# Kernel optimization log

Measured on AMD Instinct MI355X. Metric: run time of the kernel, lower is better.

Reference implementation:

```python
import jax, jax.numpy as jnp
import numpy as np

R = 1          # radius
EPS = 0.01
K = 2 * R + 1  # box kernel size


def boxfilter(x):
    """Replication-pad by R, then depthwise KxK mean filter (groups=C)."""
    xp = jnp.pad(x, ((0, 0), (0, 0), (R, R), (R, R)), mode='edge')
    c = x.shape[1]
    k = jnp.full((c, 1, K, K), 1.0 / (K * K), dtype=x.dtype)
    return jax.lax.conv_general_dilated(
        xp, k, window_strides=(1, 1), padding='VALID',
        feature_group_count=c,
        dimension_numbers=('NCHW', 'OIHW', 'NCHW'))


def _interp_axis(arr, n_in, n_out, axis):
    # bilinear with align_corners=True along one axis
    pos = jnp.linspace(0.0, n_in - 1.0, n_out)
    i0 = jnp.floor(pos).astype(jnp.int32)
    i1 = jnp.minimum(i0 + 1, n_in - 1)
    t = (pos - i0).astype(arr.dtype)
    a0 = jnp.take(arr, i0, axis=axis)
    a1 = jnp.take(arr, i1, axis=axis)
    shp = [1] * arr.ndim
    shp[axis] = n_out
    t = t.reshape(shp)
    return a0 * (1 - t) + a1 * t


def upsample_bilinear(x, H, W):
    _, _, h, w = x.shape
    x = _interp_axis(x, h, H, 2)
    x = _interp_axis(x, w, W, 3)
    return x


def setup_inputs() -> dict:
    key = jax.random.key(0)
    k1, k2, k3 = jax.random.split(key, 3)
    x_lr = jax.random.uniform(k1, (4, 3, 512, 512), dtype=jnp.float32)
    y_lr = jax.random.uniform(k2, (4, 3, 512, 512), dtype=jnp.float32)
    x_hr = jax.random.uniform(k3, (4, 3, 2048, 2048), dtype=jnp.float32)
    return {'x_lr': x_lr, 'y_lr': y_lr, 'x_hr': x_hr}


def reference(x_lr, y_lr, x_hr):
    H, W = x_hr.shape[2], x_hr.shape[3]
    mean_x = boxfilter(x_lr)
    mean_y = boxfilter(y_lr)
    cov_xy = boxfilter(x_lr * y_lr) - mean_x * mean_y
    var_x = boxfilter(x_lr * x_lr) - mean_x * mean_x
    A = cov_xy / (var_x + EPS)
    b = mean_y - A * mean_x
    mean_A = upsample_bilinear(boxfilter(A), H, W)
    mean_b = upsample_bilinear(boxfilter(b), H, W)
    res = jnp.clip(mean_A * x_hr + mean_b, 0.0, 255.0)
    return res.astype(jnp.float32)
```

## Files before the change

kernel.cpp:

```cpp
#include <hip/hip_runtime.h>

#define RAD   1
#define EPS_F 0.01f
#define LR_H  512
#define LR_W  512
#define HR_H  2048
#define HR_W  2048
#define NC    12

#define LR_PLANE (LR_H * LR_W)
#define HR_PLANE (HR_H * HR_W)
#define LR_TOTAL (NC * LR_PLANE)
#define HR_TOTAL (NC * HR_PLANE)

__global__ void __launch_bounds__(256) k_compute_Ab(
    const float* __restrict__ x, const float* __restrict__ y,
    float* __restrict__ A, float* __restrict__ b) {
    int idx = blockIdx.x * blockDim.x + threadIdx.x;
    if (idx >= LR_TOTAL) return;
    int w = idx & (LR_W - 1);
    int h = (idx >> 9) & (LR_H - 1);
    int plane = idx >> 18;
    const float* xp = x + (size_t)plane * LR_PLANE;
    const float* yp = y + (size_t)plane * LR_PLANE;

    float sx = 0.f, sy = 0.f, sxy = 0.f, sxx = 0.f;
#pragma unroll
    for (int di = -1; di <= 1; ++di) {
        int hh = min(max(h + di, 0), LR_H - 1);
        int rowoff = hh * LR_W;
#pragma unroll
        for (int dj = -1; dj <= 1; ++dj) {
            int ww = min(max(w + dj, 0), LR_W - 1);
            float xv = xp[rowoff + ww];
            float yv = yp[rowoff + ww];
            sx  += xv;
            sy  += yv;
            sxy += xv * yv;
            sxx += xv * xv;
        }
    }
    const float inv9 = 1.0f / 9.0f;
    float mx  = sx  * inv9;
    float my  = sy  * inv9;
    float cov = sxy * inv9 - mx * my;
    float var = sxx * inv9 - mx * mx;
    float Av  = cov / (var + EPS_F);
    float bv  = my - Av * mx;
    A[idx] = Av;
    b[idx] = bv;
}

__global__ void __launch_bounds__(256) k_box_Ab(
    const float* __restrict__ A, const float* __restrict__ b,
    float* __restrict__ mA, float* __restrict__ mb) {
    int idx = blockIdx.x * blockDim.x + threadIdx.x;
    if (idx >= LR_TOTAL) return;
    int w = idx & (LR_W - 1);
    int h = (idx >> 9) & (LR_H - 1);
    int plane = idx >> 18;
    const float* Ap = A + (size_t)plane * LR_PLANE;
    const float* bp = b + (size_t)plane * LR_PLANE;

    float sA = 0.f, sB = 0.f;
#pragma unroll
    for (int di = -1; di <= 1; ++di) {
        int hh = min(max(h + di, 0), LR_H - 1);
        int rowoff = hh * LR_W;
#pragma unroll
        for (int dj = -1; dj <= 1; ++dj) {
            int ww = min(max(w + dj, 0), LR_W - 1);
            sA += Ap[rowoff + ww];
            sB += bp[rowoff + ww];
        }
    }
    const float inv9 = 1.0f / 9.0f;
    mA[idx] = sA * inv9;
    mb[idx] = sB * inv9;
}

__global__ void __launch_bounds__(256) k_upsample_fuse(
    const float* __restrict__ mA, const float* __restrict__ mb,
    const float* __restrict__ xhr, float* __restrict__ out) {
    __shared__ float hA[513];
    __shared__ float hb[513];

    int bid = blockIdx.x;
    int i     = bid & (HR_H - 1);
    int plane = bid >> 11;

    const float scale = (float)(LR_H - 1) / (float)(HR_H - 1);

    float ph = i * scale;
    int   i0 = (int)ph;
    int   i1 = min(i0 + 1, LR_H - 1);
    float th = ph - (float)i0;
    float omh = 1.0f - th;

    const float* Ap = mA + (size_t)plane * LR_PLANE;
    const float* bp = mb + (size_t)plane * LR_PLANE;
    int tid = threadIdx.x;

    for (int c = tid; c < 513; c += 256) {
        int col = min(c, LR_W - 1);
        float a0 = Ap[i0 * LR_W + col];
        float a1 = Ap[i1 * LR_W + col];
        float b0 = bp[i0 * LR_W + col];
        float b1 = bp[i1 * LR_W + col];
        hA[c] = a0 * omh + a1 * th;
        hb[c] = b0 * omh + b1 * th;
    }
    __syncthreads();

    const float* xrow = xhr + (size_t)plane * HR_PLANE + (size_t)i * HR_W;
    float*       orow = out + (size_t)plane * HR_PLANE + (size_t)i * HR_W;

#pragma unroll
    for (int g = 0; g < 2; ++g) {
        int j = (tid + g * 256) * 4;
        const float4 xv = *(const float4*)(xrow + j);
        float xin[4] = {xv.x, xv.y, xv.z, xv.w};
        float r[4];
#pragma unroll
        for (int k = 0; k < 4; ++k) {
            float pw = (float)(j + k) * scale;
            int   j0 = (int)pw;
            float tw = pw - (float)j0;
            float omw = 1.0f - tw;
            float a  = hA[j0] * omw + hA[j0 + 1] * tw;
            float bb = hb[j0] * omw + hb[j0 + 1] * tw;
            float v  = a * xin[k] + bb;
            r[k] = fminf(fmaxf(v, 0.0f), 255.0f);
        }
        float4 o;
        o.x = r[0]; o.y = r[1]; o.z = r[2]; o.w = r[3];
        *(float4*)(orow + j) = o;
    }
}

extern "C" void kernel_launch(void* const* d_in, const int* in_sizes, int n_in,
                              void* d_out, int out_size, void* d_ws, size_t ws_size,
                              hipStream_t stream) {
    const float* x_lr = (const float*)d_in[0];
    const float* y_lr = (const float*)d_in[1];
    const float* x_hr = (const float*)d_in[2];
    float* out = (float*)d_out;

    float* A  = (float*)d_ws;
    float* b  = A  + LR_TOTAL;
    float* mA = b  + LR_TOTAL;
    float* mb = mA + LR_TOTAL;

    {
        int threads = 256;
        int blocks = (LR_TOTAL + threads - 1) / threads;
        k_compute_Ab<<<blocks, threads, 0, stream>>>(x_lr, y_lr, A, b);
        k_box_Ab<<<blocks, threads, 0, stream>>>(A, b, mA, mb);
    }
    {
        int threads = 256;
        int blocks = NC * HR_H;
        k_upsample_fuse<<<blocks, threads, 0, stream>>>(mA, mb, x_hr, out);
    }
}
```

Baseline: 373.6 us.

## Fuse LR coefficient computation and second box filter into one tiled kernel

Replaces the two low-resolution kernels with a single kernel that loads a 36x36 haloed tile of x and y into shared memory, computes A and b for a 34x34 region, then box-filters them from shared memory to write mean_A and mean_b. This removes the global round trip of the intermediate A and b arrays and one kernel launch. In exchange it recomputes halo values per tile and adds shared-memory staging and barriers.

```diff
diff --git a/kernel.cpp b/kernel.cpp
--- a/kernel.cpp
+++ b/kernel.cpp
@@ -13,70 +13,91 @@
 #define LR_TOTAL (NC * LR_PLANE)
 #define HR_TOTAL (NC * HR_PLANE)
 
-__global__ void __launch_bounds__(256) k_compute_Ab(
+#define TILE 32
+#define XT   (TILE + 4)
+#define XSTR (XT + 1)
+#define AT   (TILE + 2)
+#define ASTR (AT + 1)
+
+__global__ void __launch_bounds__(256) k_fused_lr(
     const float* __restrict__ x, const float* __restrict__ y,
-    float* __restrict__ A, float* __restrict__ b) {
-    int idx = blockIdx.x * blockDim.x + threadIdx.x;
-    if (idx >= LR_TOTAL) return;
-    int w = idx & (LR_W - 1);
-    int h = (idx >> 9) & (LR_H - 1);
-    int plane = idx >> 18;
-    const float* xp = x + (size_t)plane * LR_PLANE;
-    const float* yp = y + (size_t)plane * LR_PLANE;
+    float* __restrict__ mA, float* __restrict__ mb) {
+    __shared__ float xs[XT * XSTR];
+    __shared__ float ys[XT * XSTR];
+    __shared__ float As[AT * ASTR];
+    __shared__ float Bs[AT * ASTR];
 
-    float sx = 0.f, sy = 0.f, sxy = 0.f, sxx = 0.f;
+    int bid = blockIdx.x;
+    int p   = bid >> 8;
+    int rem = bid & 255;
+    int ty  = rem >> 4, tx = rem & 15;
+    int oy  = ty * TILE, ox = tx * TILE;
+    const float* xp = x + (size_t)p * LR_PLANE;
+    const float* yp = y + (size_t)p * LR_PLANE;
+    int tid = threadIdx.x;
+
+    for (int i = tid; i < XT * XT; i += 256) {
+        int r  = i / XT, c = i - r * XT;
+        int gr = min(max(oy + r - 2, 0), LR_H - 1);
+        int gc = min(max(ox + c - 2, 0), LR_W - 1);
+        xs[r * XSTR + c] = xp[gr * LR_W + gc];
+        ys[r * XSTR + c] = yp[gr * LR_W + gc];
+    }
+    __syncthreads();
+
+    for (int i = tid; i < AT * AT; i += 256) {
+        int k  = i / AT, c = i - k * AT;
+        int q  = min(max(oy + k - 1, 0), LR_H - 1);
+        int pc = min(max(ox + c - 1, 0), LR_W - 1);
+        int rows[3] = { max(q - 1, 0)         - oy + 2,
+                        q                     - oy + 2,
+                        min(q + 1, LR_H - 1)  - oy + 2 };
+        int cols[3] = { max(pc - 1, 0)        - ox + 2,
+                        pc                    - ox + 2,
+                        min(pc + 1, LR_W - 1) - ox + 2 };
+        float sx = 0.f, sy = 0.f, sxy = 0.f, sxx = 0.f;
 #pragma unroll
-    for (int di = -1; di <= 1; ++di) {
-        int hh = min(max(h + di, 0), LR_H - 1);
-        int rowoff = hh * LR_W;
+        for (int a = 0; a < 3; ++a) {
+            int ro = rows[a] * XSTR;
 #pragma unroll
-        for (int dj = -1; dj <= 1; ++dj) {
-            int ww = min(max(w + dj, 0), LR_W - 1);
-            float xv = xp[rowoff + ww];
-            float yv = yp[rowoff + ww];
-            sx  += xv;
-            sy  += yv;
-            sxy += xv * yv;
-            sxx += xv * xv;
+            for (int b2 = 0; b2 < 3; ++b2) {
+                float xv = xs[ro + cols[b2]];
+                float yv = ys[ro + cols[b2]];
+                sx  += xv;
+                sy  += yv;
+                sxy += xv * yv;
+                sxx += xv * xv;
+            }
         }
+        const float inv9 = 1.0f / 9.0f;
+        float mx  = sx * inv9;
+        float my  = sy * inv9;
+        float cov = sxy * inv9 - mx * my;
+        float var = sxx * inv9 - mx * mx;
+        float Av  = cov / (var + EPS_F);
+        As[k * ASTR + c] = Av;
+        Bs[k * ASTR + c] = my - Av * mx;
     }
-    const float inv9 = 1.0f / 9.0f;
-    float mx  = sx  * inv9;
-    float my  = sy  * inv9;
-    float cov = sxy * inv9 - mx * my;
-    float var = sxx * inv9 - mx * mx;
-    float Av  = cov / (var + EPS_F);
-    float bv  = my - Av * mx;
-    A[idx] = Av;
-    b[idx] = bv;
-}
+    __syncthreads();
 
-__global__ void __launch_bounds__(256) k_box_Ab(
-    const float* __restrict__ A, const float* __restrict__ b,
-    float* __restrict__ mA, float* __restrict__ mb) {
-    int idx = blockIdx.x * blockDim.x + threadIdx.x;
-    if (idx >= LR_TOTAL) return;
-    int w = idx & (LR_W - 1);
-    int h = (idx >> 9) & (LR_H - 1);
-    int plane = idx >> 18;
-    const float* Ap = A + (size_t)plane * LR_PLANE;
-    const float* bp = b + (size_t)plane * LR_PLANE;
-
-    float sA = 0.f, sB = 0.f;
+    float* mAp = mA + (size_t)p * LR_PLANE;
+    float* mbp = mb + (size_t)p * LR_PLANE;
+    for (int i = tid; i < TILE * TILE; i += 256) {
+        int r = i >> 5, c = i & 31;
+        float sA = 0.f, sB = 0.f;
 #pragma unroll
-    for (int di = -1; di <= 1; ++di) {
-        int hh = min(max(h + di, 0), LR_H - 1);
-        int rowoff = hh * LR_W;
+        for (int a = 0; a < 3; ++a) {
+            int ro = (r + a) * ASTR + c;
 #pragma unroll
-        for (int dj = -1; dj <= 1; ++dj) {
-            int ww = min(max(w + dj, 0), LR_W - 1);
-            sA += Ap[rowoff + ww];
-            sB += bp[rowoff + ww];
+            for (int b2 = 0; b2 < 3; ++b2) {
+                sA += As[ro + b2];
+                sB += Bs[ro + b2];
+            }
         }
+        const float inv9 = 1.0f / 9.0f;
+        mAp[(size_t)(oy + r) * LR_W + (ox + c)] = sA * inv9;
+        mbp[(size_t)(oy + r) * LR_W + (ox + c)] = sB * inv9;
     }
-    const float inv9 = 1.0f / 9.0f;
-    mA[idx] = sA * inv9;
-    mb[idx] = sB * inv9;
 }
 
 __global__ void __launch_bounds__(256) k_upsample_fuse(
@@ -146,16 +167,13 @@
     const float* x_hr = (const float*)d_in[2];
     float* out = (float*)d_out;
 
-    float* A  = (float*)d_ws;
-    float* b  = A  + LR_TOTAL;
-    float* mA = b  + LR_TOTAL;
+    float* mA = (float*)d_ws;
     float* mb = mA + LR_TOTAL;
 
     {
         int threads = 256;
-        int blocks = (LR_TOTAL + threads - 1) / threads;
-        k_compute_Ab<<<blocks, threads, 0, stream>>>(x_lr, y_lr, A, b);
-        k_box_Ab<<<blocks, threads, 0, stream>>>(A, b, mA, mb);
+        int blocks = NC * 16 * 16;
+        k_fused_lr<<<blocks, threads, 0, stream>>>(x_lr, y_lr, mA, mb);
     }
     {
         int threads = 256;
```

Result: faster. 365.4 us (-2.2%).

## Fuse box filters, A/b computation and upsample into one tiled kernel

Applied to the files above, without the earlier changes.

Replaces the three kernels with one kernel. Each block handles four HR output rows and recomputes the needed low-res rows of A, b and their box means in shared memory from a 7-row halo of x and y. This removes the workspace round trips and two kernel launches, but recomputes overlapping low-res rows across neighbouring blocks and uses about 48KB of LDS per block. The block index is also swizzled across planes.

```diff
diff --git a/kernel.cpp b/kernel.cpp
--- a/kernel.cpp
+++ b/kernel.cpp
@@ -1,6 +1,5 @@
 #include <hip/hip_runtime.h>
 
-#define RAD   1
 #define EPS_F 0.01f
 #define LR_H  512
 #define LR_W  512
@@ -10,131 +9,152 @@
 
 #define LR_PLANE (LR_H * LR_W)
 #define HR_PLANE (HR_H * HR_W)
-#define LR_TOTAL (NC * LR_PLANE)
-#define HR_TOTAL (NC * HR_PLANE)
 
-__global__ void __launch_bounds__(256) k_compute_Ab(
+#define XROWS 7
+#define XW    516
+#define XSTR  517
+#define AROWS 5
+#define AW    514
+#define ASTR  515
+#define MROWS 3
+#define MW    513
+#define MSTR  513
+
+#define SMEM_FLOATS 12388
+
+__global__ void __launch_bounds__(256) k_guided(
     const float* __restrict__ x, const float* __restrict__ y,
-    float* __restrict__ A, float* __restrict__ b) {
-    int idx = blockIdx.x * blockDim.x + threadIdx.x;
-    if (idx >= LR_TOTAL) return;
-    int w = idx & (LR_W - 1);
-    int h = (idx >> 9) & (LR_H - 1);
-    int plane = idx >> 18;
-    const float* xp = x + (size_t)plane * LR_PLANE;
-    const float* yp = y + (size_t)plane * LR_PLANE;
-
-    float sx = 0.f, sy = 0.f, sxy = 0.f, sxx = 0.f;
-#pragma unroll
-    for (int di = -1; di <= 1; ++di) {
-        int hh = min(max(h + di, 0), LR_H - 1);
-        int rowoff = hh * LR_W;
-#pragma unroll
-        for (int dj = -1; dj <= 1; ++dj) {
-            int ww = min(max(w + dj, 0), LR_W - 1);
-            float xv = xp[rowoff + ww];
-            float yv = yp[rowoff + ww];
-            sx  += xv;
-            sy  += yv;
-            sxy += xv * yv;
-            sxx += xv * xv;
-        }
-    }
-    const float inv9 = 1.0f / 9.0f;
-    float mx  = sx  * inv9;
-    float my  = sy  * inv9;
-    float cov = sxy * inv9 - mx * my;
-    float var = sxx * inv9 - mx * mx;
-    float Av  = cov / (var + EPS_F);
-    float bv  = my - Av * mx;
-    A[idx] = Av;
-    b[idx] = bv;
-}
-
-__global__ void __launch_bounds__(256) k_box_Ab(
-    const float* __restrict__ A, const float* __restrict__ b,
-    float* __restrict__ mA, float* __restrict__ mb) {
-    int idx = blockIdx.x * blockDim.x + threadIdx.x;
-    if (idx >= LR_TOTAL) return;
-    int w = idx & (LR_W - 1);
-    int h = (idx >> 9) & (LR_H - 1);
-    int plane = idx >> 18;
-    const float* Ap = A + (size_t)plane * LR_PLANE;
-    const float* bp = b + (size_t)plane * LR_PLANE;
-
-    float sA = 0.f, sB = 0.f;
-#pragma unroll
-    for (int di = -1; di <= 1; ++di) {
-        int hh = min(max(h + di, 0), LR_H - 1);
-        int rowoff = hh * LR_W;
-#pragma unroll
-        for (int dj = -1; dj <= 1; ++dj) {
-            int ww = min(max(w + dj, 0), LR_W - 1);
-            sA += Ap[rowoff + ww];
-            sB += bp[rowoff + ww];
-        }
-    }
-    const float inv9 = 1.0f / 9.0f;
-    mA[idx] = sA * inv9;
-    mb[idx] = sB * inv9;
-}
-
-__global__ void __launch_bounds__(256) k_upsample_fuse(
-    const float* __restrict__ mA, const float* __restrict__ mb,
     const float* __restrict__ xhr, float* __restrict__ out) {
-    __shared__ float hA[513];
-    __shared__ float hb[513];
-
-    int bid = blockIdx.x;
-    int i     = bid & (HR_H - 1);
-    int plane = bid >> 11;
+    __shared__ float smem[SMEM_FLOATS];
+    float* xs  = smem;
+    float* ys  = smem + 3619;
+    float* As  = smem + 7238;
+    float* Bs  = smem + 9813;
+    float* mAs = smem;
+    float* mbs = smem + 1539;
 
     const float scale = (float)(LR_H - 1) / (float)(HR_H - 1);
 
-    float ph = i * scale;
-    int   i0 = (int)ph;
-    int   i1 = min(i0 + 1, LR_H - 1);
-    float th = ph - (float)i0;
-    float omh = 1.0f - th;
+    int bid = blockIdx.x;
+    int lin = (bid & 7) * 768 + (bid >> 3);
+    int p   = lin >> 9;
+    int rb  = lin & 511;
+    int R   = (int)((float)(4 * rb) * scale);
 
-    const float* Ap = mA + (size_t)plane * LR_PLANE;
-    const float* bp = mb + (size_t)plane * LR_PLANE;
     int tid = threadIdx.x;
+    const float* xp = x + (size_t)p * LR_PLANE;
+    const float* yp = y + (size_t)p * LR_PLANE;
 
-    for (int c = tid; c < 513; c += 256) {
-        int col = min(c, LR_W - 1);
-        float a0 = Ap[i0 * LR_W + col];
-        float a1 = Ap[i1 * LR_W + col];
-        float b0 = bp[i0 * LR_W + col];
-        float b1 = bp[i1 * LR_W + col];
-        hA[c] = a0 * omh + a1 * th;
-        hb[c] = b0 * omh + b1 * th;
+    for (int r = 0; r < XROWS; ++r) {
+        int gr = min(max(R - 2 + r, 0), LR_H - 1);
+        const float* xrow = xp + gr * LR_W;
+        const float* yrow = yp + gr * LR_W;
+        for (int c = tid; c < XW; c += 256) {
+            int gc = min(max(c - 2, 0), LR_W - 1);
+            xs[r * XSTR + c] = xrow[gc];
+            ys[r * XSTR + c] = yrow[gc];
+        }
     }
     __syncthreads();
 
-    const float* xrow = xhr + (size_t)plane * HR_PLANE + (size_t)i * HR_W;
-    float*       orow = out + (size_t)plane * HR_PLANE + (size_t)i * HR_W;
+    for (int q = 0; q < AROWS; ++q) {
+        int qq = min(max(R - 1 + q, 0), LR_H - 1);
+        int rbase = (qq - R + 2) * XSTR;
+        for (int j = tid; j < AW; j += 256) {
+            int pc = min(max(j - 1, 0), LR_W - 1);
+            int cbase = rbase + pc + 2;
+            float sx = 0.f, sy = 0.f, sxy = 0.f, sxx = 0.f;
+#pragma unroll
+            for (int d = -1; d <= 1; ++d) {
+                int ro = cbase + d * XSTR;
+#pragma unroll
+                for (int e = -1; e <= 1; ++e) {
+                    float xv = xs[ro + e];
+                    float yv = ys[ro + e];
+                    sx  += xv;
+                    sy  += yv;
+                    sxy += xv * yv;
+                    sxx += xv * xv;
+                }
+            }
+            const float inv9 = 1.0f / 9.0f;
+            float mx  = sx * inv9;
+            float my  = sy * inv9;
+            float cov = sxy * inv9 - mx * my;
+            float var = sxx * inv9 - mx * mx;
+            float Av  = cov / (var + EPS_F);
+            As[q * ASTR + j] = Av;
+            Bs[q * ASTR + j] = my - Av * mx;
+        }
+    }
+    __syncthreads();
+
+    for (int t = 0; t < MROWS; ++t) {
+        int rr = min(R + t, LR_H - 1);
+        int q0 = max(rr - 1, 0) - R + 1;
+        int q1 = rr - R + 1;
+        int q2 = min(rr + 1, LR_H - 1) - R + 1;
+        for (int j = tid; j < MW; j += 256) {
+            int cc = min(j, LR_W - 1);
+            int c0 = cc;
+            int r0 = q0 * ASTR + c0;
+            int r1 = q1 * ASTR + c0;
+            int r2 = q2 * ASTR + c0;
+            float sA = 0.f, sB = 0.f;
+            sA += As[r0] + As[r0 + 1] + As[r0 + 2];
+            sA += As[r1] + As[r1 + 1] + As[r1 + 2];
+            sA += As[r2] + As[r2 + 1] + As[r2 + 2];
+            sB += Bs[r0] + Bs[r0 + 1] + Bs[r0 + 2];
+            sB += Bs[r1] + Bs[r1 + 1] + Bs[r1 + 2];
+            sB += Bs[r2] + Bs[r2 + 1] + Bs[r2 + 2];
+            const float inv9 = 1.0f / 9.0f;
+            mAs[t * MSTR + j] = sA * inv9;
+            mbs[t * MSTR + j] = sB * inv9;
+        }
+    }
+    __syncthreads();
+
+    const size_t hrbase = (size_t)p * HR_PLANE;
+#pragma unroll
+    for (int k = 0; k < 4; ++k) {
+        int i = 4 * rb + k;
+        float ph = (float)i * scale;
+        int   i0 = (int)ph;
+        float th = ph - (float)i0;
+        int   i1 = min(i0 + 1, LR_H - 1);
+        float omh = 1.0f - th;
+        const float* a0 = mAs + (i0 - R) * MSTR;
+        const float* a1 = mAs + (i1 - R) * MSTR;
+        const float* b0 = mbs + (i0 - R) * MSTR;
+        const float* b1 = mbs + (i1 - R) * MSTR;
+        const float* xrow = xhr + hrbase + (size_t)i * HR_W;
+        float*       orow = out + hrbase + (size_t)i * HR_W;
 
 #pragma unroll
-    for (int g = 0; g < 2; ++g) {
-        int j = (tid + g * 256) * 4;
-        const float4 xv = *(const float4*)(xrow + j);
-        float xin[4] = {xv.x, xv.y, xv.z, xv.w};
-        float r[4];
+        for (int g = 0; g < 2; ++g) {
+            int j = (tid + g * 256) * 4;
+            const float4 xv = *(const float4*)(xrow + j);
+            float xin[4] = {xv.x, xv.y, xv.z, xv.w};
+            float r[4];
 #pragma unroll
-        for (int k = 0; k < 4; ++k) {
-            float pw = (float)(j + k) * scale;
-            int   j0 = (int)pw;
-            float tw = pw - (float)j0;
-            float omw = 1.0f - tw;
-            float a  = hA[j0] * omw + hA[j0 + 1] * tw;
-            float bb = hb[j0] * omw + hb[j0 + 1] * tw;
-            float v  = a * xin[k] + bb;
-            r[k] = fminf(fmaxf(v, 0.0f), 255.0f);
+            for (int kk = 0; kk < 4; ++kk) {
+                float pw = (float)(j + kk) * scale;
+                int   j0 = (int)pw;
+                float tw = pw - (float)j0;
+                float omw = 1.0f - tw;
+                float ha0 = a0[j0]     * omh + a1[j0]     * th;
+                float ha1 = a0[j0 + 1] * omh + a1[j0 + 1] * th;
+                float hb0 = b0[j0]     * omh + b1[j0]     * th;
+                float hb1 = b0[j0 + 1] * omh + b1[j0 + 1] * th;
+                float a  = ha0 * omw + ha1 * tw;
+                float bb = hb0 * omw + hb1 * tw;
+                float v  = a * xin[kk] + bb;
+                r[kk] = fminf(fmaxf(v, 0.0f), 255.0f);
+            }
+            float4 o;
+            o.x = r[0]; o.y = r[1]; o.z = r[2]; o.w = r[3];
+            *(float4*)(orow + j) = o;
         }
-        float4 o;
-        o.x = r[0]; o.y = r[1]; o.z = r[2]; o.w = r[3];
-        *(float4*)(orow + j) = o;
     }
 }
 
@@ -145,21 +165,9 @@
     const float* y_lr = (const float*)d_in[1];
     const float* x_hr = (const float*)d_in[2];
     float* out = (float*)d_out;
+    (void)d_ws; (void)ws_size;
 
-    float* A  = (float*)d_ws;
-    float* b  = A  + LR_TOTAL;
-    float* mA = b  + LR_TOTAL;
-    float* mb = mA + LR_TOTAL;
-
-    {
-        int threads = 256;
-        int blocks = (LR_TOTAL + threads - 1) / threads;
-        k_compute_Ab<<<blocks, threads, 0, stream>>>(x_lr, y_lr, A, b);
-        k_box_Ab<<<blocks, threads, 0, stream>>>(A, b, mA, mb);
-    }
-    {
-        int threads = 256;
-        int blocks = NC * HR_H;
-        k_upsample_fuse<<<blocks, threads, 0, stream>>>(mA, mb, x_hr, out);
-    }
+    int threads = 256;
+    int blocks  = NC * (HR_H / 4);
+    k_guided<<<blocks, threads, 0, stream>>>(x_lr, y_lr, x_hr, out);
 }
```

Result: slower. 431.8 us (+15.6%).
